# Kernel optimization log

Measured on AMD Instinct MI355X. Metric: run time of the kernel, lower is better.

Reference implementation:

```python
import jax, jax.numpy as jnp
import numpy as np

N = 50000      # total atoms in batched graph
E = 800000     # edges
IN = 128       # in_feats
OUT = 64       # out_feats (per GAT head)
H = 4          # num_heads
NEG_SLOPE = 0.2
BN_EPS = 1e-5


def setup_inputs() -> dict:
    key = jax.random.key(0)
    ks = jax.random.split(key, 16)
    s = 0.1  # keep activations well-scaled
    return {
        "node_feats": jax.random.normal(ks[0], (N, IN), jnp.float32),
        "W_fc":       jax.random.normal(ks[1], (IN, H * OUT), jnp.float32) * s,
        "attn_l":     jax.random.normal(ks[2], (H, OUT), jnp.float32) * s,
        "attn_r":     jax.random.normal(ks[3], (H, OUT), jnp.float32) * s,
        "gat_res_w":  jax.random.normal(ks[4], (IN, H * OUT), jnp.float32) * s,
        "gat_bias":   jax.random.normal(ks[5], (H * OUT,), jnp.float32) * s,
        "conv_w":     jax.random.normal(ks[6], (1, H, 1), jnp.float32) * s,
        "conv_b":     jax.random.normal(ks[7], (1,), jnp.float32) * s,
        "res_w":      jax.random.normal(ks[8], (IN, OUT), jnp.float32) * s,
        "res_b":      jax.random.normal(ks[9], (OUT,), jnp.float32) * s,
        "bn_gamma":   jnp.ones((OUT,), jnp.float32),
        "bn_beta":    jnp.zeros((OUT,), jnp.float32),
        "src":        jax.random.randint(ks[10], (E,), 0, N, jnp.int32),
        "dst":        jax.random.randint(ks[11], (E,), 0, N, jnp.int32),
        "etype":      0,
    }


def reference(node_feats, W_fc, attn_l, attn_r, gat_res_w, gat_bias,
              conv_w, conv_b, res_w, res_b, bn_gamma, bn_beta,
              src, dst, etype):
    # ---- GATConv (DGL semantics, eval mode: no dropout) ----
    h = (node_feats @ W_fc).reshape(-1, H, OUT)            # [N,H,D]
    el = jnp.sum(h * attn_l, axis=-1)                      # [N,H]
    er = jnp.sum(h * attn_r, axis=-1)                      # [N,H]
    e = jax.nn.leaky_relu(el[src] + er[dst], NEG_SLOPE)    # [E,H]
    # segment softmax over incoming edges of each dst node
    m = jax.ops.segment_max(e, dst, num_segments=N)        # [N,H]
    m = jnp.where(jnp.isfinite(m), m, 0.0)                 # empty segments
    a = jnp.exp(e - m[dst])                                # [E,H]
    ssum = jax.ops.segment_sum(a, dst, num_segments=N)     # [N,H]
    alpha = a / (ssum[dst] + 1e-16)                        # [E,H]
    # weighted aggregation: rst[v] = sum_{(u->v)} alpha * h[u]
    rst = jax.ops.segment_sum(alpha[:, :, None] * h[src], dst, num_segments=N)  # [N,H,D]
    # GAT residual (in != H*OUT -> linear res_fc, no bias) + bias + activation
    rst = rst + (node_feats @ gat_res_w).reshape(-1, H, OUT) + gat_bias.reshape(H, OUT)
    rst = jax.nn.relu(rst)                                 # [N,H,D]
    # ---- Conv1d(4 -> 1, kernel=1): weighted head merge ----
    y = jnp.einsum("nhd,h->nd", rst, conv_w[0, :, 0]) + conv_b[0]  # [N,D]
    # ---- outer residual ----
    y = y + jax.nn.relu(node_feats @ res_w + res_b)
    # ---- BatchNorm1d (training-style batch stats) ----
    mean = jnp.mean(y, axis=0)
    var = jnp.var(y, axis=0)
    return (y - mean) / jnp.sqrt(var + BN_EPS) * bn_gamma + bn_beta
```

## Files before the change

### kernel.cpp

```cpp
#include <hip/hip_runtime.h>

#define IN_F   128
#define OUTD   64
#define HOUT   256
#define NEG_SLOPE 0.2f
#define BN_EPS 1e-5f
#define HISTB  256

typedef __attribute__((ext_vector_type(8))) short bf16x8;
typedef __attribute__((ext_vector_type(4))) float f32x4;
typedef __attribute__((ext_vector_type(2))) float f32x2;

__device__ __forceinline__ unsigned short f2bf(float f) {
    union { float f; unsigned u; } v; v.f = f;
    unsigned r = (v.u + 0x7FFF + ((v.u >> 16) & 1)) >> 16;
    return (unsigned short)r;
}
__device__ __forceinline__ float bf2f(unsigned short h) {
    union { unsigned u; float f; } v; v.u = ((unsigned)h) << 16;
    return v.f;
}
__device__ __forceinline__ float u2f(unsigned u) {
    union { unsigned u; float f; } v; v.u = u;
    return v.f;
}
__device__ __forceinline__ unsigned f2u(float f) {
    union { float f; unsigned u; } v; v.f = f;
    return v.u;
}

__device__ __forceinline__ int b2idx(int c, int k) {
    int tt, j;
    if (c < 256)      { tt = (c >> 4) & 3;                     j = c >> 6; }
    else if (c < 512) { int cc = c - 256; tt = 4 + ((cc >> 4) & 3); j = cc >> 6; }
    else if (c < 576) { int cc = c - 512; tt = 8;              j = cc >> 4; }
    else              { tt = 9;                                j = 0; }
    int n15 = c & 15;
    int ks = k >> 5, qd = (k >> 3) & 3, kk = k & 7;
    return ((((tt * 4 + j) * 4 + ks) * 64) + qd * 16 + n15) * 8 + kk;
}

__global__ __launch_bounds__(256) void k0_pack(
    const float* __restrict__ W_fc, const float* __restrict__ W_gres,
    const float* __restrict__ W_res,
    const float* __restrict__ attn_l, const float* __restrict__ attn_r,
    unsigned short* __restrict__ Btg2)
{
    int bid = blockIdx.x, t = threadIdx.x;
    if (bid < 288) {
        int idx = bid * 256 + t;
        int c = idx >> 7, k = idx & 127;
        float v;
        if (c < 256)      v = W_fc[k * HOUT + c];
        else if (c < 512) v = W_gres[k * HOUT + (c - 256)];
        else              v = W_res[k * OUTD + (c - 512)];
        Btg2[b2idx(c, k)] = f2bf(v);
        return;
    }
    for (int p = t; p < 512; p += 256) {
        int h = p >> 7, k = p & 127;
        float sl = 0.f, sr = 0.f;
        for (int d = 0; d < 64; ++d) {
            float wv = W_fc[k * HOUT + h * 64 + d];
            sl += wv * attn_l[h * 64 + d];
            sr += wv * attn_r[h * 64 + d];
        }
        Btg2[b2idx(576 + h, k)] = f2bf(sl);
        Btg2[b2idx(580 + h, k)] = f2bf(sr);
    }
    for (int p = t; p < 8 * 128; p += 256) {
        int c = 584 + (p >> 7), k = p & 127;
        Btg2[b2idx(c, k)] = 0;
    }
}

__global__ __launch_bounds__(256) void k1_gemm(
    const float* __restrict__ A, const unsigned short* __restrict__ Btg2,
    const float* __restrict__ gat_bias, const float* __restrict__ res_b,
    const int* __restrict__ dst, int* __restrict__ degree, int* __restrict__ rank,
    unsigned char* __restrict__ Hh8, unsigned char* __restrict__ Hr8,
    unsigned short* __restrict__ Rres,
    float* __restrict__ el, float* __restrict__ er,
    int N, int E, int Gblocks)
{
    int t = threadIdx.x;

    if (blockIdx.x >= Gblocks) {
        int ht = (blockIdx.x - Gblocks) * 256 + t;
        for (int e = ht; e < E; e += HISTB * 256)
            rank[e] = atomicAdd(degree + dst[e], 1);
        return;
    }

    int w = t >> 6, lane = t & 63, quad = lane >> 4, n15 = lane & 15;
    int gw = blockIdx.x * 4 + w;
    int T = (N + 15) / 16;
    if (gw >= T) return;

    int m0 = gw * 16;
    bool full = (m0 + 16 <= N);
    int lofs = (quad * 16 + n15) * 8;

    bf16x8 af[4];
    {
        int r = m0 + n15;
#pragma unroll
        for (int ks = 0; ks < 4; ++ks) {
            float4 v0 = make_float4(0.f, 0.f, 0.f, 0.f), v1 = v0;
            if (r < N) {
                const float* ap = A + (size_t)r * IN_F + ks * 32 + quad * 8;
                v0 = *(const float4*)ap;
                v1 = *(const float4*)(ap + 4);
            }
            bf16x8 o;
            o[0] = f2bf(v0.x); o[1] = f2bf(v0.y); o[2] = f2bf(v0.z); o[3] = f2bf(v0.w);
            o[4] = f2bf(v1.x); o[5] = f2bf(v1.y); o[6] = f2bf(v1.z); o[7] = f2bf(v1.w);
            af[ks] = o;
        }
    }

#pragma unroll
    for (int s = 0; s < 4; ++s) {
        bf16x8 bfr[4][4];
#pragma unroll
        for (int ks = 0; ks < 4; ++ks)
#pragma unroll
            for (int j = 0; j < 4; ++j)
                bfr[ks][j] = *(const bf16x8*)(Btg2 + ((s * 16 + j * 4 + ks) << 9) + lofs);
        f32x4 acc[4] = {};
#pragma unroll
        for (int ks = 0; ks < 4; ++ks)
#pragma unroll
            for (int j = 0; j < 4; ++j)
                acc[j] = __builtin_amdgcn_mfma_f32_16x16x32_bf16(af[ks], bfr[ks][j], acc[j], 0, 0, 0);
#pragma unroll
        for (int reg = 0; reg < 4; ++reg) {
            int r = m0 + quad * 4 + reg;
            if (full || r < N) {
                unsigned pk = (unsigned)__builtin_amdgcn_cvt_pk_fp8_f32(acc[0][reg], acc[1][reg], 0, false);
                pk = (unsigned)__builtin_amdgcn_cvt_pk_fp8_f32(acc[2][reg], acc[3][reg], (int)pk, true);
                *(unsigned*)(Hh8 + ((size_t)r << 8) + (s * 16 + n15) * 4) = pk;
            }
        }
    }

#pragma unroll
    for (int s = 0; s < 4; ++s) {
        bf16x8 bfr[4][4];
#pragma unroll
        for (int ks = 0; ks < 4; ++ks)
#pragma unroll
            for (int j = 0; j < 4; ++j)
                bfr[ks][j] = *(const bf16x8*)(Btg2 + (((4 + s) * 16 + j * 4 + ks) << 9) + lofs);
        f32x4 acc[4] = {};
#pragma unroll
        for (int ks = 0; ks < 4; ++ks)
#pragma unroll
            for (int j = 0; j < 4; ++j)
                acc[j] = __builtin_amdgcn_mfma_f32_16x16x32_bf16(af[ks], bfr[ks][j], acc[j], 0, 0, 0);
        float b0 = gat_bias[0 * 64 + s * 16 + n15];
        float b1 = gat_bias[1 * 64 + s * 16 + n15];
        float b2 = gat_bias[2 * 64 + s * 16 + n15];
        float b3 = gat_bias[3 * 64 + s * 16 + n15];
#pragma unroll
        for (int reg = 0; reg < 4; ++reg) {
            int r = m0 + quad * 4 + reg;
            if (full || r < N) {
                unsigned pk = (unsigned)__builtin_amdgcn_cvt_pk_fp8_f32(acc[0][reg] + b0, acc[1][reg] + b1, 0, false);
                pk = (unsigned)__builtin_amdgcn_cvt_pk_fp8_f32(acc[2][reg] + b2, acc[3][reg] + b3, (int)pk, true);
                *(unsigned*)(Hr8 + ((size_t)r << 8) + (s * 16 + n15) * 4) = pk;
            }
        }
    }

    {
        bf16x8 bfr[4][4];
#pragma unroll
        for (int ks = 0; ks < 4; ++ks)
#pragma unroll
            for (int j = 0; j < 4; ++j)
                bfr[ks][j] = *(const bf16x8*)(Btg2 + ((8 * 16 + j * 4 + ks) << 9) + lofs);
        f32x4 acc[4] = {};
#pragma unroll
        for (int ks = 0; ks < 4; ++ks)
#pragma unroll
            for (int j = 0; j < 4; ++j)
                acc[j] = __builtin_amdgcn_mfma_f32_16x16x32_bf16(af[ks], bfr[ks][j], acc[j], 0, 0, 0);
#pragma unroll
        for (int reg = 0; reg < 4; ++reg) {
            int r = m0 + quad * 4 + reg;
            if (full || r < N) {
#pragma unroll
                for (int j = 0; j < 4; ++j)
                    Rres[(size_t)r * OUTD + j * 16 + n15] = f2bf(acc[j][reg] + res_b[j * 16 + n15]);
            }
        }
    }

    {
        bf16x8 b4[4];
#pragma unroll
        for (int ks = 0; ks < 4; ++ks)
            b4[ks] = *(const bf16x8*)(Btg2 + ((9 * 16 + ks) << 9) + lofs);
        f32x4 acc2 = {};
#pragma unroll
        for (int ks = 0; ks < 4; ++ks)
            acc2 = __builtin_amdgcn_mfma_f32_16x16x32_bf16(af[ks], b4[ks], acc2, 0, 0, 0);
#pragma unroll
        for (int reg = 0; reg < 4; ++reg) {
            int r = m0 + quad * 4 + reg;
            if ((full || r < N) && n15 < 8) {
                float v = acc2[reg];
                if (n15 < 4) el[(size_t)r * 4 + n15] = v;
                else         er[(size_t)r * 4 + (n15 - 4)] = v;
            }
        }
    }
}

__global__ __launch_bounds__(256) void scanA_kernel(const int* __restrict__ degree,
                                                    int* __restrict__ excl,
                                                    int* __restrict__ blocksum, int N) {
    __shared__ int sm[256];
    int t = threadIdx.x;
    int i = blockIdx.x * 256 + t;
    int d = (i < N) ? degree[i] : 0;
    sm[t] = d; __syncthreads();
    for (int off = 1; off < 256; off <<= 1) {
        int v = (t >= off) ? sm[t - off] : 0;
        __syncthreads();
        sm[t] += v;
        __syncthreads();
    }
    if (i < N) excl[i] = sm[t] - d;
    if (t == 255) blocksum[blockIdx.x] = sm[255];
}

__global__ __launch_bounds__(256) void scatter_kernel(
    const int* __restrict__ src, const int* __restrict__ dst,
    const int* __restrict__ rank, const int* __restrict__ excl,
    const int* __restrict__ blocksum, int* __restrict__ base,
    unsigned* __restrict__ usrc_sorted, int E, int nb) {
    __shared__ int sm[256];
    __shared__ int base_lds[256];
    int t = threadIdx.x;
    int d0 = (t < nb) ? blocksum[t] : 0;
    sm[t] = d0; __syncthreads();
    for (int off = 1; off < 256; off <<= 1) {
        int v = (t >= off) ? sm[t - off] : 0;
        __syncthreads();
        sm[t] += v;
        __syncthreads();
    }
    base_lds[t] = sm[t] - d0;
    if (blockIdx.x == 0) base[t] = sm[t] - d0;
    __syncthreads();

    int e = blockIdx.x * 256 + t;
    if (e >= E) return;
    int d = dst[e];
    int p = excl[d] + base_lds[d >> 8] + rank[e];
    usrc_sorted[p] = (unsigned)src[e] << 8;
}

__global__ __launch_bounds__(256) void agg_kernel(
    const unsigned char* __restrict__ Hh8, const unsigned char* __restrict__ Hr8,
    const unsigned short* __restrict__ Rres, const float* __restrict__ el,
    const float* __restrict__ er,
    const int* __restrict__ excl, const int* __restrict__ base,
    const unsigned* __restrict__ usrc_sorted,
    const float* __restrict__ conv_w, const float* __restrict__ conv_b,
    float* __restrict__ y, float* __restrict__ bnsum8, float* __restrict__ bnsq8,
    int N, int E)
{
    __shared__ float smem[256];
    __shared__ float smem2[256];
    int t = threadIdx.x;
    int wave = t >> 6, lane = t & 63;
    int v = blockIdx.x * 4 + wave;

    float yv = 0.f;
    if (v < N) {
        int b  = excl[v] + base[v >> 8];
        int e2 = (v + 1 < N) ? (excl[v + 1] + base[(v + 1) >> 8]) : E;
        int deg = e2 - b;

        float4 rv = *(const float4*)(er + (size_t)v * 4);
        const unsigned char* hbase = Hh8 + lane * 4;
        float a0 = 0.f, a1 = 0.f, a2 = 0.f, a3 = 0.f;
        float p0 = 0.f, p1 = 0.f, p2 = 0.f, p3 = 0.f;

        for (int i0 = 0; i0 < deg; i0 += 64) {
            int j = i0 + lane;
            unsigned ux = 0;
            float s0 = 0.f, s1 = 0.f, s2 = 0.f, s3 = 0.f;
            if (j < deg) {
                ux = usrc_sorted[b + j];
                float4 l = *(const float4*)(el + ((size_t)(ux >> 8)) * 4);
                float x;
                x = l.x + rv.x; x = x > 0.f ? x : NEG_SLOPE * x; s0 = __expf(x);
                x = l.y + rv.y; x = x > 0.f ? x : NEG_SLOPE * x; s1 = __expf(x);
                x = l.z + rv.z; x = x > 0.f ? x : NEG_SLOPE * x; s2 = __expf(x);
                x = l.w + rv.w; x = x > 0.f ? x : NEG_SLOPE * x; s3 = __expf(x);
                p0 += s0; p1 += s1; p2 += s2; p3 += s3;
            }
            int cl = deg - i0; if (cl > 64) cl = 64;
            int jj = 0;
            for (; jj + 3 < cl; jj += 4) {
                unsigned u_[4], hv[4];
                float w0[4], w1[4], w2[4], w3[4];
#pragma unroll
                for (int k = 0; k < 4; ++k) {
                    u_[k] = (unsigned)__builtin_amdgcn_readlane((int)ux, jj + k);
                    w0[k] = u2f((unsigned)__builtin_amdgcn_readlane((int)f2u(s0), jj + k));
                    w1[k] = u2f((unsigned)__builtin_amdgcn_readlane((int)f2u(s1), jj + k));
                    w2[k] = u2f((unsigned)__builtin_amdgcn_readlane((int)f2u(s2), jj + k));
                    w3[k] = u2f((unsigned)__builtin_amdgcn_readlane((int)f2u(s3), jj + k));
                }
#pragma unroll
                for (int k = 0; k < 4; ++k)
                    hv[k] = *(const unsigned*)(hbase + u_[k]);
#pragma unroll
                for (int k = 0; k < 4; ++k) {
                    f32x2 lo = __builtin_amdgcn_cvt_pk_f32_fp8(hv[k], false);
                    f32x2 hi = __builtin_amdgcn_cvt_pk_f32_fp8(hv[k], true);
                    a0 += w0[k] * lo.x;
                    a1 += w1[k] * lo.y;
                    a2 += w2[k] * hi.x;
                    a3 += w3[k] * hi.y;
                }
            }
            for (; jj < cl; ++jj) {
                unsigned uA = (unsigned)__builtin_amdgcn_readlane((int)ux, jj);
                float w0 = u2f((unsigned)__builtin_amdgcn_readlane((int)f2u(s0), jj));
                float w1 = u2f((unsigned)__builtin_amdgcn_readlane((int)f2u(s1), jj));
                float w2 = u2f((unsigned)__builtin_amdgcn_readlane((int)f2u(s2), jj));
                float w3 = u2f((unsigned)__builtin_amdgcn_readlane((int)f2u(s3), jj));
                unsigned hvA = *(const unsigned*)(hbase + uA);
                f32x2 lo = __builtin_amdgcn_cvt_pk_f32_fp8(hvA, false);
                f32x2 hi = __builtin_amdgcn_cvt_pk_f32_fp8(hvA, true);
                a0 += w0 * lo.x;
                a1 += w1 * lo.y;
                a2 += w2 * hi.x;
                a3 += w3 * hi.y;
            }
        }
#pragma unroll
        for (int off = 1; off < 64; off <<= 1) {
            p0 += __shfl_xor(p0, off); p1 += __shfl_xor(p1, off);
            p2 += __shfl_xor(p2, off); p3 += __shfl_xor(p3, off);
        }
        float r0 = 1.f / (p0 + 1e-16f), r1 = 1.f / (p1 + 1e-16f);
        float r2 = 1.f / (p2 + 1e-16f), r3 = 1.f / (p3 + 1e-16f);

        unsigned hr = *(const unsigned*)(Hr8 + ((size_t)v << 8) + lane * 4);
        f32x2 rlo = __builtin_amdgcn_cvt_pk_f32_fp8(hr, false);
        f32x2 rhi = __builtin_amdgcn_cvt_pk_f32_fp8(hr, true);
        float resv = bf2f(Rres[(size_t)v * OUTD + lane]);
        yv = conv_b[0] + (resv > 0.f ? resv : 0.f);
        float tt;
        tt = a0 * r0 + rlo.x; tt = tt > 0.f ? tt : 0.f; yv += conv_w[0] * tt;
        tt = a1 * r1 + rlo.y; tt = tt > 0.f ? tt : 0.f; yv += conv_w[1] * tt;
        tt = a2 * r2 + rhi.x; tt = tt > 0.f ? tt : 0.f; yv += conv_w[2] * tt;
        tt = a3 * r3 + rhi.y; tt = tt > 0.f ? tt : 0.f; yv += conv_w[3] * tt;
        y[(size_t)v * OUTD + lane] = yv;
    }

    smem[t] = yv;
    smem2[t] = yv * yv;
    __syncthreads();
    if (t < 64) {
        float s = smem[t] + smem[t + 64] + smem[t + 128] + smem[t + 192];
        float q = smem2[t] + smem2[t + 64] + smem2[t + 128] + smem2[t + 192];
        int c = (blockIdx.x & 7) << 6;
        atomicAdd(bnsum8 + c + t, s);
        atomicAdd(bnsq8 + c + t, q);
    }
}

__global__ __launch_bounds__(256) void norm_kernel(
    const float* __restrict__ y,
    const float* __restrict__ bnsum8, const float* __restrict__ bnsq8,
    const float* __restrict__ gamma, const float* __restrict__ beta,
    float* __restrict__ out, int total4, float invN) {
    __shared__ float scale[64], shift[64];
    int t = threadIdx.x;
    if (t < 64) {
        float s = 0.f, q = 0.f;
#pragma unroll
        for (int c = 0; c < 8; ++c) { s += bnsum8[c * 64 + t]; q += bnsq8[c * 64 + t]; }
        float mean = s * invN;
        float var = q * invN - mean * mean;
        float sc = gamma[t] * rsqrtf(var + BN_EPS);
        scale[t] = sc;
        shift[t] = beta[t] - mean * sc;
    }
    __syncthreads();
    int idx = blockIdx.x * blockDim.x + t;
    if (idx >= total4) return;
    float4 v = *(const float4*)(y + (size_t)idx * 4);
    int d = (idx * 4) & 63;
    float4 o;
    o.x = v.x * scale[d + 0] + shift[d + 0];
    o.y = v.y * scale[d + 1] + shift[d + 1];
    o.z = v.z * scale[d + 2] + shift[d + 2];
    o.w = v.w * scale[d + 3] + shift[d + 3];
    *(float4*)(out + (size_t)idx * 4) = o;
}

extern "C" void kernel_launch(void* const* d_in, const int* in_sizes, int n_in,
                              void* d_out, int out_size, void* d_ws, size_t ws_size,
                              hipStream_t stream) {
    const float* node_feats = (const float*)d_in[0];
    const float* W_fc       = (const float*)d_in[1];
    const float* attn_l     = (const float*)d_in[2];
    const float* attn_r     = (const float*)d_in[3];
    const float* gat_res_w  = (const float*)d_in[4];
    const float* gat_bias   = (const float*)d_in[5];
    const float* conv_w     = (const float*)d_in[6];
    const float* conv_b     = (const float*)d_in[7];
    const float* res_w      = (const float*)d_in[8];
    const float* res_b      = (const float*)d_in[9];
    const float* bn_gamma   = (const float*)d_in[10];
    const float* bn_beta    = (const float*)d_in[11];
    const int*   src        = (const int*)d_in[12];
    const int*   dst        = (const int*)d_in[13];

    const int N = in_sizes[0] / IN_F;
    const int E = in_sizes[12];
    const int nb = (N + 255) / 256;
    const int T = (N + 15) / 16;
    const int Gblocks = (T + 3) / 4;

    char* ws = (char*)d_ws;
    size_t off = 0;
    auto alloc = [&](size_t bytes) -> void* {
        void* p = (void*)(ws + off);
        off += (bytes + 255) & ~(size_t)255;
        return p;
    };

    int*   degree  = (int*)alloc((size_t)N * 4);
    float* bnsum8  = (float*)alloc(8 * 64 * 4);
    float* bnsq8   = (float*)alloc(8 * 64 * 4);
    size_t zero_bytes = off;
    int*            rank        = (int*)alloc((size_t)E * 4);
    int*            excl        = (int*)alloc((size_t)N * 4);
    int*            blocksum    = (int*)alloc(256 * 4);
    int*            base        = (int*)alloc(256 * 4);
    unsigned*       usrc_sorted = (unsigned*)alloc((size_t)E * 4);
    unsigned short* Btg2        = (unsigned short*)alloc((size_t)10 * 16 * 512 * 2);
    unsigned char*  Hh8         = (unsigned char*)alloc((size_t)N * 256);
    unsigned char*  Hr8         = (unsigned char*)alloc((size_t)N * 256);
    unsigned short* Rres        = (unsigned short*)alloc((size_t)N * OUTD * 2);
    float*          el          = (float*)alloc((size_t)N * 4 * 4);
    float*          er          = (float*)alloc((size_t)N * 4 * 4);
    float*          y           = (float*)alloc((size_t)N * OUTD * 4);
    (void)ws_size; (void)n_in; (void)out_size;

    hipMemsetAsync(d_ws, 0, zero_bytes, stream);

    k0_pack<<<289, 256, 0, stream>>>(W_fc, gat_res_w, res_w, attn_l, attn_r, Btg2);
    k1_gemm<<<Gblocks + HISTB, 256, 0, stream>>>(node_feats, Btg2, gat_bias, res_b,
                                                 dst, degree, rank, Hh8, Hr8, Rres,
                                                 el, er, N, E, Gblocks);
    scanA_kernel<<<nb, 256, 0, stream>>>(degree, excl, blocksum, N);
    scatter_kernel<<<(E + 255) / 256, 256, 0, stream>>>(src, dst, rank, excl, blocksum,
                                                        base, usrc_sorted, E, nb);
    agg_kernel<<<(N + 3) / 4, 256, 0, stream>>>(Hh8, Hr8, Rres, el, er, excl, base,
                                                usrc_sorted, conv_w, conv_b, y,
                                                bnsum8, bnsq8, N, E);
    norm_kernel<<<(N * OUTD / 4 + 255) / 256, 256, 0, stream>>>(y, bnsum8, bnsq8,
                                                                bn_gamma, bn_beta, (float*)d_out,
                                                                N * OUTD / 4, 1.f / (float)N);
}
```

Baseline: 224.6 us.

## Fuse the six-kernel pipeline into one cooperative persistent kernel with grid syncs

```diff
diff --git a/kernel.cpp b/kernel.cpp
--- a/kernel.cpp
+++ b/kernel.cpp
@@ -1,4 +1,7 @@
 #include <hip/hip_runtime.h>
+#include <hip/hip_cooperative_groups.h>
+
+namespace cg = cooperative_groups;
 
 #define IN_F   128
 #define OUTD   64
@@ -40,13 +43,10 @@
     return ((((tt * 4 + j) * 4 + ks) * 64) + qd * 16 + n15) * 8 + kk;
 }
 
-__global__ __launch_bounds__(256) void k0_pack(
-    const float* __restrict__ W_fc, const float* __restrict__ W_gres,
-    const float* __restrict__ W_res,
-    const float* __restrict__ attn_l, const float* __restrict__ attn_r,
-    unsigned short* __restrict__ Btg2)
+__device__ __forceinline__ void pack_body(int bid, int t,
+    const float* W_fc, const float* W_gres, const float* W_res,
+    const float* attn_l, const float* attn_r, unsigned short* Btg2)
 {
-    int bid = blockIdx.x, t = threadIdx.x;
     if (bid < 288) {
         int idx = bid * 256 + t;
         int c = idx >> 7, k = idx & 127;
@@ -57,8 +57,8 @@
         Btg2[b2idx(c, k)] = f2bf(v);
         return;
     }
-    for (int p = t; p < 512; p += 256) {
-        int h = p >> 7, k = p & 127;
+    for (int q = t; q < 512; q += 256) {
+        int h = q >> 7, k = q & 127;
         float sl = 0.f, sr = 0.f;
         for (int d = 0; d < 64; ++d) {
             float wv = W_fc[k * HOUT + h * 64 + d];
@@ -68,35 +68,17 @@
         Btg2[b2idx(576 + h, k)] = f2bf(sl);
         Btg2[b2idx(580 + h, k)] = f2bf(sr);
     }
-    for (int p = t; p < 8 * 128; p += 256) {
-        int c = 584 + (p >> 7), k = p & 127;
-        Btg2[b2idx(c, k)] = 0;
-    }
-}
-
-__global__ __launch_bounds__(256) void k1_gemm(
-    const float* __restrict__ A, const unsigned short* __restrict__ Btg2,
-    const float* __restrict__ gat_bias, const float* __restrict__ res_b,
-    const int* __restrict__ dst, int* __restrict__ degree, int* __restrict__ rank,
-    unsigned char* __restrict__ Hh8, unsigned char* __restrict__ Hr8,
-    unsigned short* __restrict__ Rres,
-    float* __restrict__ el, float* __restrict__ er,
-    int N, int E, int Gblocks)
+    for (int q = t; q < 8 * 128; q += 256)
+        Btg2[b2idx(584 + (q >> 7), q & 127)] = 0;
+}
+
+__device__ __forceinline__ void gemm_tile_body(int gw, int t,
+    const float* A, const unsigned short* Btg2,
+    const float* gat_bias, const float* res_b,
+    unsigned char* Hh8, unsigned char* Hr8, unsigned short* Rres,
+    float* el, float* er, int N)
 {
-    int t = threadIdx.x;
-
-    if (blockIdx.x >= Gblocks) {
-        int ht = (blockIdx.x - Gblocks) * 256 + t;
-        for (int e = ht; e < E; e += HISTB * 256)
-            rank[e] = atomicAdd(degree + dst[e], 1);
-        return;
-    }
-
-    int w = t >> 6, lane = t & 63, quad = lane >> 4, n15 = lane & 15;
-    int gw = blockIdx.x * 4 + w;
-    int T = (N + 15) / 16;
-    if (gw >= T) return;
-
+    int lane = t & 63, quad = lane >> 4, n15 = lane & 15;
     int m0 = gw * 16;
     bool full = (m0 + 16 <= N);
     int lofs = (quad * 16 + n15) * 8;
@@ -143,7 +125,6 @@
             }
         }
     }
-
 #pragma unroll
     for (int s = 0; s < 4; ++s) {
         bf16x8 bfr[4][4];
@@ -172,7 +153,6 @@
             }
         }
     }
-
     {
         bf16x8 bfr[4][4];
 #pragma unroll
@@ -196,7 +176,6 @@
             }
         }
     }
-
     {
         bf16x8 b4[4];
 #pragma unroll
@@ -209,13 +188,253 @@
 #pragma unroll
         for (int reg = 0; reg < 4; ++reg) {
             int r = m0 + quad * 4 + reg;
-            if ((full || r < N) && n15 < 8) {
+            if ((r < N) && n15 < 8) {
                 float v = acc2[reg];
                 if (n15 < 4) el[(size_t)r * 4 + n15] = v;
                 else         er[(size_t)r * 4 + (n15 - 4)] = v;
             }
         }
     }
+}
+
+__device__ __forceinline__ float agg_node_body(int v, int lane,
+    const unsigned char* Hh8, const unsigned char* Hr8, const unsigned short* Rres,
+    const float* el, const float* er, const unsigned* usrc,
+    int b, int deg, float cb, float cw0, float cw1, float cw2, float cw3,
+    float* y)
+{
+    float4 rv = *(const float4*)(er + (size_t)v * 4);
+    const unsigned char* hbase = Hh8 + lane * 4;
+    float a0 = 0.f, a1 = 0.f, a2 = 0.f, a3 = 0.f;
+    float p0 = 0.f, p1 = 0.f, p2 = 0.f, p3 = 0.f;
+
+    for (int i0 = 0; i0 < deg; i0 += 64) {
+        int j = i0 + lane;
+        unsigned ux = 0;
+        float s0 = 0.f, s1 = 0.f, s2 = 0.f, s3 = 0.f;
+        if (j < deg) {
+            ux = usrc[b + j];
+            float4 l = *(const float4*)(el + ((size_t)(ux >> 8)) * 4);
+            float x;
+            x = l.x + rv.x; x = x > 0.f ? x : NEG_SLOPE * x; s0 = __expf(x);
+            x = l.y + rv.y; x = x > 0.f ? x : NEG_SLOPE * x; s1 = __expf(x);
+            x = l.z + rv.z; x = x > 0.f ? x : NEG_SLOPE * x; s2 = __expf(x);
+            x = l.w + rv.w; x = x > 0.f ? x : NEG_SLOPE * x; s3 = __expf(x);
+            p0 += s0; p1 += s1; p2 += s2; p3 += s3;
+        }
+        int cl = deg - i0; if (cl > 64) cl = 64;
+        int jj = 0;
+        for (; jj + 3 < cl; jj += 4) {
+            unsigned u_[4], hv[4];
+            float w0[4], w1[4], w2[4], w3[4];
+#pragma unroll
+            for (int k = 0; k < 4; ++k) {
+                u_[k] = (unsigned)__builtin_amdgcn_readlane((int)ux, jj + k);
+                w0[k] = u2f((unsigned)__builtin_amdgcn_readlane((int)f2u(s0), jj + k));
+                w1[k] = u2f((unsigned)__builtin_amdgcn_readlane((int)f2u(s1), jj + k));
+                w2[k] = u2f((unsigned)__builtin_amdgcn_readlane((int)f2u(s2), jj + k));
+                w3[k] = u2f((unsigned)__builtin_amdgcn_readlane((int)f2u(s3), jj + k));
+            }
+#pragma unroll
+            for (int k = 0; k < 4; ++k)
+                hv[k] = *(const unsigned*)(hbase + u_[k]);
+#pragma unroll
+            for (int k = 0; k < 4; ++k) {
+                f32x2 lo = __builtin_amdgcn_cvt_pk_f32_fp8(hv[k], false);
+                f32x2 hi = __builtin_amdgcn_cvt_pk_f32_fp8(hv[k], true);
+                a0 += w0[k] * lo.x;
+                a1 += w1[k] * lo.y;
+                a2 += w2[k] * hi.x;
+                a3 += w3[k] * hi.y;
+            }
+        }
+        for (; jj < cl; ++jj) {
+            unsigned uA = (unsigned)__builtin_amdgcn_readlane((int)ux, jj);
+            float w0 = u2f((unsigned)__builtin_amdgcn_readlane((int)f2u(s0), jj));
+            float w1 = u2f((unsigned)__builtin_amdgcn_readlane((int)f2u(s1), jj));
+            float w2 = u2f((unsigned)__builtin_amdgcn_readlane((int)f2u(s2), jj));
+            float w3 = u2f((unsigned)__builtin_amdgcn_readlane((int)f2u(s3), jj));
+            unsigned hvA = *(const unsigned*)(hbase + uA);
+            f32x2 lo = __builtin_amdgcn_cvt_pk_f32_fp8(hvA, false);
+            f32x2 hi = __builtin_amdgcn_cvt_pk_f32_fp8(hvA, true);
+            a0 += w0 * lo.x;
+            a1 += w1 * lo.y;
+            a2 += w2 * hi.x;
+            a3 += w3 * hi.y;
+        }
+    }
+#pragma unroll
+    for (int off = 1; off < 64; off <<= 1) {
+        p0 += __shfl_xor(p0, off); p1 += __shfl_xor(p1, off);
+        p2 += __shfl_xor(p2, off); p3 += __shfl_xor(p3, off);
+    }
+    float r0 = 1.f / (p0 + 1e-16f), r1 = 1.f / (p1 + 1e-16f);
+    float r2 = 1.f / (p2 + 1e-16f), r3 = 1.f / (p3 + 1e-16f);
+
+    unsigned hr = *(const unsigned*)(Hr8 + ((size_t)v << 8) + lane * 4);
+    f32x2 rlo = __builtin_amdgcn_cvt_pk_f32_fp8(hr, false);
+    f32x2 rhi = __builtin_amdgcn_cvt_pk_f32_fp8(hr, true);
+    float resv = bf2f(Rres[(size_t)v * OUTD + lane]);
+    float yv = cb + (resv > 0.f ? resv : 0.f);
+    float tt;
+    tt = a0 * r0 + rlo.x; tt = tt > 0.f ? tt : 0.f; yv += cw0 * tt;
+    tt = a1 * r1 + rlo.y; tt = tt > 0.f ? tt : 0.f; yv += cw1 * tt;
+    tt = a2 * r2 + rhi.x; tt = tt > 0.f ? tt : 0.f; yv += cw2 * tt;
+    tt = a3 * r3 + rhi.y; tt = tt > 0.f ? tt : 0.f; yv += cw3 * tt;
+    y[(size_t)v * OUTD + lane] = yv;
+    return yv;
+}
+
+struct KParams {
+    const float *A, *W_fc, *attn_l, *attn_r, *W_gres, *gat_bias;
+    const float *conv_w, *conv_b, *W_res, *res_b, *bn_gamma, *bn_beta;
+    const int *src, *dst;
+    int *degree, *rank, *excl, *blocksum;
+    unsigned *usrc;
+    unsigned short *Btg2;
+    unsigned char *Hh8, *Hr8;
+    unsigned short *Rres;
+    float *el, *er, *y, *bnsum8, *bnsq8, *out;
+    int N, E, nb, T;
+    float invN;
+};
+
+__global__ __launch_bounds__(256, 4) void fused(KParams p)
+{
+    __shared__ int   sm_i[256];
+    __shared__ int   base_lds[256];
+    __shared__ float fA[256];
+    __shared__ float fB[256];
+
+    cg::grid_group grid = cg::this_grid();
+    int bid = blockIdx.x, t = threadIdx.x;
+    int nblk = (int)gridDim.x;
+    int w = t >> 6, lane = t & 63;
+
+    if (bid <= 288) {
+        pack_body(bid, t, p.W_fc, p.W_gres, p.W_res, p.attn_l, p.attn_r, p.Btg2);
+    } else {
+        int stride = (nblk - 289) << 8;
+        for (int e = ((bid - 289) << 8) + t; e < p.E; e += stride)
+            p.rank[e] = atomicAdd(p.degree + p.dst[e], 1);
+    }
+    grid.sync();
+
+    for (int c = bid; c < p.nb; c += nblk) {
+        int i = (c << 8) + t;
+        int d = (i < p.N) ? p.degree[i] : 0;
+        sm_i[t] = d; __syncthreads();
+        for (int off = 1; off < 256; off <<= 1) {
+            int v = (t >= off) ? sm_i[t - off] : 0;
+            __syncthreads();
+            sm_i[t] += v;
+            __syncthreads();
+        }
+        if (i < p.N) p.excl[i] = sm_i[t] - d;
+        if (t == 255) p.blocksum[c] = sm_i[255];
+        __syncthreads();
+    }
+    grid.sync();
+
+    {
+        int d0 = (t < p.nb) ? p.blocksum[t] : 0;
+        sm_i[t] = d0; __syncthreads();
+        for (int off = 1; off < 256; off <<= 1) {
+            int v = (t >= off) ? sm_i[t - off] : 0;
+            __syncthreads();
+            sm_i[t] += v;
+            __syncthreads();
+        }
+        base_lds[t] = sm_i[t] - d0;
+        __syncthreads();
+    }
+    for (int e = (bid << 8) + t; e < p.E; e += (nblk << 8)) {
+        int d = p.dst[e];
+        int pos = p.excl[d] + base_lds[d >> 8] + p.rank[e];
+        p.usrc[pos] = (unsigned)p.src[e] << 8;
+    }
+    for (int gw = bid * 4 + w; gw < p.T; gw += nblk * 4)
+        gemm_tile_body(gw, t, p.A, p.Btg2, p.gat_bias, p.res_b,
+                       p.Hh8, p.Hr8, p.Rres, p.el, p.er, p.N);
+    grid.sync();
+
+    float bn_s = 0.f, bn_q = 0.f;
+    {
+        float cb = p.conv_b[0];
+        float cw0 = p.conv_w[0], cw1 = p.conv_w[1], cw2 = p.conv_w[2], cw3 = p.conv_w[3];
+        for (int v = bid * 4 + w; v < p.N; v += nblk * 4) {
+            int b  = p.excl[v] + base_lds[v >> 8];
+            int e2 = (v + 1 < p.N) ? (p.excl[v + 1] + base_lds[(v + 1) >> 8]) : p.E;
+            float yv = agg_node_body(v, lane, p.Hh8, p.Hr8, p.Rres, p.el, p.er,
+                                     p.usrc, b, e2 - b, cb, cw0, cw1, cw2, cw3, p.y);
+            bn_s += yv; bn_q += yv * yv;
+        }
+    }
+    fA[t] = bn_s;
+    fB[t] = bn_q;
+    __syncthreads();
+    if (t < 64) {
+        float s = fA[t] + fA[t + 64] + fA[t + 128] + fA[t + 192];
+        float q = fB[t] + fB[t + 64] + fB[t + 128] + fB[t + 192];
+        int c = (bid & 7) << 6;
+        atomicAdd(p.bnsum8 + c + t, s);
+        atomicAdd(p.bnsq8 + c + t, q);
+    }
+    grid.sync();
+
+    if (t < 64) {
+        float s = 0.f, q = 0.f;
+#pragma unroll
+        for (int c = 0; c < 8; ++c) { s += p.bnsum8[c * 64 + t]; q += p.bnsq8[c * 64 + t]; }
+        float mean = s * p.invN;
+        float var = q * p.invN - mean * mean;
+        float sc = p.bn_gamma[t] * rsqrtf(var + BN_EPS);
+        fA[t] = sc;
+        fB[t] = p.bn_beta[t] - mean * sc;
+    }
+    __syncthreads();
+    int total4 = p.N * OUTD / 4;
+    for (int idx = (bid << 8) + t; idx < total4; idx += (nblk << 8)) {
+        float4 v = *(const float4*)(p.y + (size_t)idx * 4);
+        int d = (idx * 4) & 63;
+        float4 o;
+        o.x = v.x * fA[d + 0] + fB[d + 0];
+        o.y = v.y * fA[d + 1] + fB[d + 1];
+        o.z = v.z * fA[d + 2] + fB[d + 2];
+        o.w = v.w * fA[d + 3] + fB[d + 3];
+        *(float4*)(p.out + (size_t)idx * 4) = o;
+    }
+}
+
+__global__ __launch_bounds__(256) void k0_pack(
+    const float* __restrict__ W_fc, const float* __restrict__ W_gres,
+    const float* __restrict__ W_res,
+    const float* __restrict__ attn_l, const float* __restrict__ attn_r,
+    unsigned short* __restrict__ Btg2)
+{
+    pack_body(blockIdx.x, threadIdx.x, W_fc, W_gres, W_res, attn_l, attn_r, Btg2);
+}
+
+__global__ __launch_bounds__(256) void k1_gemm(
+    const float* __restrict__ A, const unsigned short* __restrict__ Btg2,
+    const float* __restrict__ gat_bias, const float* __restrict__ res_b,
+    const int* __restrict__ dst, int* __restrict__ degree, int* __restrict__ rank,
+    unsigned char* __restrict__ Hh8, unsigned char* __restrict__ Hr8,
+    unsigned short* __restrict__ Rres,
+    float* __restrict__ el, float* __restrict__ er,
+    int N, int E, int Gblocks)
+{
+    int t = threadIdx.x;
+    if (blockIdx.x >= Gblocks) {
+        int ht = (blockIdx.x - Gblocks) * 256 + t;
+        for (int e = ht; e < E; e += HISTB * 256)
+            rank[e] = atomicAdd(degree + dst[e], 1);
+        return;
+    }
+    int gw = blockIdx.x * 4 + (t >> 6);
+    int T = (N + 15) / 16;
+    if (gw >= T) return;
+    gemm_tile_body(gw, t, A, Btg2, gat_bias, res_b, Hh8, Hr8, Rres, el, er, N);
 }
 
 __global__ __launch_bounds__(256) void scanA_kernel(const int* __restrict__ degree,
@@ -255,7 +474,6 @@
     base_lds[t] = sm[t] - d0;
     if (blockIdx.x == 0) base[t] = sm[t] - d0;
     __syncthreads();
-
     int e = blockIdx.x * 256 + t;
     if (e >= E) return;
     int d = dst[e];
@@ -283,89 +501,9 @@
     if (v < N) {
         int b  = excl[v] + base[v >> 8];
         int e2 = (v + 1 < N) ? (excl[v + 1] + base[(v + 1) >> 8]) : E;
-        int deg = e2 - b;
-
-        float4 rv = *(const float4*)(er + (size_t)v * 4);
-        const unsigned char* hbase = Hh8 + lane * 4;
-        float a0 = 0.f, a1 = 0.f, a2 = 0.f, a3 = 0.f;
-        float p0 = 0.f, p1 = 0.f, p2 = 0.f, p3 = 0.f;
-
-        for (int i0 = 0; i0 < deg; i0 += 64) {
-            int j = i0 + lane;
-            unsigned ux = 0;
-            float s0 = 0.f, s1 = 0.f, s2 = 0.f, s3 = 0.f;
-            if (j < deg) {
-                ux = usrc_sorted[b + j];
-                float4 l = *(const float4*)(el + ((size_t)(ux >> 8)) * 4);
-                float x;
-                x = l.x + rv.x; x = x > 0.f ? x : NEG_SLOPE * x; s0 = __expf(x);
-                x = l.y + rv.y; x = x > 0.f ? x : NEG_SLOPE * x; s1 = __expf(x);
-                x = l.z + rv.z; x = x > 0.f ? x : NEG_SLOPE * x; s2 = __expf(x);
-                x = l.w + rv.w; x = x > 0.f ? x : NEG_SLOPE * x; s3 = __expf(x);
-                p0 += s0; p1 += s1; p2 += s2; p3 += s3;
-            }
-            int cl = deg - i0; if (cl > 64) cl = 64;
-            int jj = 0;
-            for (; jj + 3 < cl; jj += 4) {
-                unsigned u_[4], hv[4];
-                float w0[4], w1[4], w2[4], w3[4];
-#pragma unroll
-                for (int k = 0; k < 4; ++k) {
-                    u_[k] = (unsigned)__builtin_amdgcn_readlane((int)ux, jj + k);
-                    w0[k] = u2f((unsigned)__builtin_amdgcn_readlane((int)f2u(s0), jj + k));
-                    w1[k] = u2f((unsigned)__builtin_amdgcn_readlane((int)f2u(s1), jj + k));
-                    w2[k] = u2f((unsigned)__builtin_amdgcn_readlane((int)f2u(s2), jj + k));
-                    w3[k] = u2f((unsigned)__builtin_amdgcn_readlane((int)f2u(s3), jj + k));
-                }
-#pragma unroll
-                for (int k = 0; k < 4; ++k)
-                    hv[k] = *(const unsigned*)(hbase + u_[k]);
-#pragma unroll
-                for (int k = 0; k < 4; ++k) {
-                    f32x2 lo = __builtin_amdgcn_cvt_pk_f32_fp8(hv[k], false);
-                    f32x2 hi = __builtin_amdgcn_cvt_pk_f32_fp8(hv[k], true);
-                    a0 += w0[k] * lo.x;
-                    a1 += w1[k] * lo.y;
-                    a2 += w2[k] * hi.x;
-                    a3 += w3[k] * hi.y;
-                }
-            }
-            for (; jj < cl; ++jj) {
-                unsigned uA = (unsigned)__builtin_amdgcn_readlane((int)ux, jj);
-                float w0 = u2f((unsigned)__builtin_amdgcn_readlane((int)f2u(s0), jj));
-                float w1 = u2f((unsigned)__builtin_amdgcn_readlane((int)f2u(s1), jj));
-                float w2 = u2f((unsigned)__builtin_amdgcn_readlane((int)f2u(s2), jj));
-                float w3 = u2f((unsigned)__builtin_amdgcn_readlane((int)f2u(s3), jj));
-                unsigned hvA = *(const unsigned*)(hbase + uA);
-                f32x2 lo = __builtin_amdgcn_cvt_pk_f32_fp8(hvA, false);
-                f32x2 hi = __builtin_amdgcn_cvt_pk_f32_fp8(hvA, true);
-                a0 += w0 * lo.x;
-                a1 += w1 * lo.y;
-                a2 += w2 * hi.x;
-                a3 += w3 * hi.y;
-            }
-        }
-#pragma unroll
-        for (int off = 1; off < 64; off <<= 1) {
-            p0 += __shfl_xor(p0, off); p1 += __shfl_xor(p1, off);
-            p2 += __shfl_xor(p2, off); p3 += __shfl_xor(p3, off);
-        }
-        float r0 = 1.f / (p0 + 1e-16f), r1 = 1.f / (p1 + 1e-16f);
-        float r2 = 1.f / (p2 + 1e-16f), r3 = 1.f / (p3 + 1e-16f);
-
-        unsigned hr = *(const unsigned*)(Hr8 + ((size_t)v << 8) + lane * 4);
-        f32x2 rlo = __builtin_amdgcn_cvt_pk_f32_fp8(hr, false);
-        f32x2 rhi = __builtin_amdgcn_cvt_pk_f32_fp8(hr, true);
-        float resv = bf2f(Rres[(size_t)v * OUTD + lane]);
-        yv = conv_b[0] + (resv > 0.f ? resv : 0.f);
-        float tt;
-        tt = a0 * r0 + rlo.x; tt = tt > 0.f ? tt : 0.f; yv += conv_w[0] * tt;
-        tt = a1 * r1 + rlo.y; tt = tt > 0.f ? tt : 0.f; yv += conv_w[1] * tt;
-        tt = a2 * r2 + rhi.x; tt = tt > 0.f ? tt : 0.f; yv += conv_w[2] * tt;
-        tt = a3 * r3 + rhi.y; tt = tt > 0.f ? tt : 0.f; yv += conv_w[3] * tt;
-        y[(size_t)v * OUTD + lane] = yv;
-    }
-
+        yv = agg_node_body(v, lane, Hh8, Hr8, Rres, el, er, usrc_sorted,
+                           b, e2 - b, conv_b[0], conv_w[0], conv_w[1], conv_w[2], conv_w[3], y);
+    }
     smem[t] = yv;
     smem2[t] = yv * yv;
     __syncthreads();
@@ -411,21 +549,6 @@
 extern "C" void kernel_launch(void* const* d_in, const int* in_sizes, int n_in,
                               void* d_out, int out_size, void* d_ws, size_t ws_size,
                               hipStream_t stream) {
-    const float* node_feats = (const float*)d_in[0];
-    const float* W_fc       = (const float*)d_in[1];
-    const float* attn_l     = (const float*)d_in[2];
-    const float* attn_r     = (const float*)d_in[3];
-    const float* gat_res_w  = (const float*)d_in[4];
-    const float* gat_bias   = (const float*)d_in[5];
-    const float* conv_w     = (const float*)d_in[6];
-    const float* conv_b     = (const float*)d_in[7];
-    const float* res_w      = (const float*)d_in[8];
-    const float* res_b      = (const float*)d_in[9];
-    const float* bn_gamma   = (const float*)d_in[10];
-    const float* bn_beta    = (const float*)d_in[11];
-    const int*   src        = (const int*)d_in[12];
-    const int*   dst        = (const int*)d_in[13];
-
     const int N = in_sizes[0] / IN_F;
     const int E = in_sizes[12];
     const int nb = (N + 255) / 256;
@@ -460,17 +583,68 @@
 
     hipMemsetAsync(d_ws, 0, zero_bytes, stream);
 
-    k0_pack<<<289, 256, 0, stream>>>(W_fc, gat_res_w, res_w, attn_l, attn_r, Btg2);
-    k1_gemm<<<Gblocks + HISTB, 256, 0, stream>>>(node_feats, Btg2, gat_bias, res_b,
-                                                 dst, degree, rank, Hh8, Hr8, Rres,
-                                                 el, er, N, E, Gblocks);
-    scanA_kernel<<<nb, 256, 0, stream>>>(degree, excl, blocksum, N);
-    scatter_kernel<<<(E + 255) / 256, 256, 0, stream>>>(src, dst, rank, excl, blocksum,
-                                                        base, usrc_sorted, E, nb);
-    agg_kernel<<<(N + 3) / 4, 256, 0, stream>>>(Hh8, Hr8, Rres, el, er, excl, base,
-                                                usrc_sorted, conv_w, conv_b, y,
-                                                bnsum8, bnsq8, N, E);
-    norm_kernel<<<(N * OUTD / 4 + 255) / 256, 256, 0, stream>>>(y, bnsum8, bnsq8,
-                                                                bn_gamma, bn_beta, (float*)d_out,
-                                                                N * OUTD / 4, 1.f / (float)N);
-}
+    static int s_nblk = -1;
+    if (s_nblk < 0) {
+        int occ = 0, cus = 0;
+        if (hipOccupancyMaxActiveBlocksPerMultiprocessor(&occ, (const void*)fused, 256, 0) != hipSuccess)
+            occ = 0;
+        if (hipDeviceGetAttribute(&cus, hipDeviceAttributeMultiprocessorCount, 0) != hipSuccess)
+            cus = 0;
+        long total = (long)occ * (long)cus;
+        if (total > 2048) total = 2048;
+        s_nblk = (total >= 320) ? (int)total : 0;
+    }
+
+    bool ok = false;
+    if (s_nblk > 0) {
+        KParams kp;
+        kp.A        = (const float*)d_in[0];
+        kp.W_fc     = (const float*)d_in[1];
+        kp.attn_l   = (const float*)d_in[2];
+        kp.attn_r   = (const float*)d_in[3];
+        kp.W_gres   = (const float*)d_in[4];
+        kp.gat_bias = (const float*)d_in[5];
+        kp.conv_w   = (const float*)d_in[6];
+        kp.conv_b   = (const float*)d_in[7];
+        kp.W_res    = (const float*)d_in[8];
+        kp.res_b    = (const float*)d_in[9];
+        kp.bn_gamma = (const float*)d_in[10];
+        kp.bn_beta  = (const float*)d_in[11];
+        kp.src      = (const int*)d_in[12];
+        kp.dst      = (const int*)d_in[13];
+        kp.degree = degree; kp.rank = rank; kp.excl = excl; kp.blocksum = blocksum;
+        kp.usrc = usrc_sorted; kp.Btg2 = Btg2; kp.Hh8 = Hh8; kp.Hr8 = Hr8;
+        kp.Rres = Rres; kp.el = el; kp.er = er; kp.y = y;
+        kp.bnsum8 = bnsum8; kp.bnsq8 = bnsq8; kp.out = (float*)d_out;
+        kp.N = N; kp.E = E; kp.nb = nb; kp.T = T;
+        kp.invN = 1.f / (float)N;
+        void* args[] = { (void*)&kp };
+        hipError_t err = hipLaunchCooperativeKernel((const void*)fused, dim3(s_nblk),
+                                                    dim3(256), args, 0, stream);
+        if (err == hipSuccess) ok = true;
+        else s_nblk = 0;
+    }
+
+    if (!ok) {
+        k0_pack<<<289, 256, 0, stream>>>((const float*)d_in[1], (const float*)d_in[4],
+                                         (const float*)d_in[8], (const float*)d_in[2],
+                                         (const float*)d_in[3], Btg2);
+        k1_gemm<<<Gblocks + HISTB, 256, 0, stream>>>((const float*)d_in[0], Btg2,
+                                                     (const float*)d_in[5], (const float*)d_in[9],
+                                                     (const int*)d_in[13], degree, rank,
+                                                     Hh8, Hr8, Rres, el, er, N, E, Gblocks);
+        scanA_kernel<<<nb, 256, 0, stream>>>(degree, excl, blocksum, N);
+        scatter_kernel<<<(E + 255) / 256, 256, 0, stream>>>((const int*)d_in[12],
+                                                            (const int*)d_in[13], rank, excl,
+                                                            blocksum, base, usrc_sorted, E, nb);
+        agg_kernel<<<(N + 3) / 4, 256, 0, stream>>>(Hh8, Hr8, Rres, el, er, excl, base,
+                                                    usrc_sorted, (const float*)d_in[6],
+                                                    (const float*)d_in[7], y,
+                                                    bnsum8, bnsq8, N, E);
+        norm_kernel<<<(N * OUTD / 4 + 255) / 256, 256, 0, stream>>>(y, bnsum8, bnsq8,
+                                                                    (const float*)d_in[10],
+                                                                    (const float*)d_in[11],
+                                                                    (float*)d_out,
+                                                                    N * OUTD / 4, 1.f / (float)N);
+    }
+}
```

Measured after the change: 625.1 us. +178.3%, slower.
